# Performance work log

Measured on AMD Instinct MI355X. Metric: run time of the kernel, lower is better.

The kernel has to match this reference:

```python
import jax, jax.numpy as jnp
import numpy as np

HEADS, DIM_HEAD, LANDMARKS, PINV_ITERS = 8, 64, 256, 6
DIM, IN_DIM = 512, 1536
LN_EPS = 1e-5
SCALE = DIM_HEAD ** -0.5


def layernorm(x, g, b):
    mu = x.mean(-1, keepdims=True)
    var = jnp.mean((x - mu) ** 2, axis=-1, keepdims=True)
    return (x - mu) * jax.lax.rsqrt(var + LN_EPS) * g + b


def moore_penrose_pinv(x, iters=PINV_ITERS):
    # Newton-Schulz iteration exactly as in lucidrains/nystrom-attention
    ax = jnp.abs(x)
    z = jnp.swapaxes(x, -1, -2) / (jnp.max(ax.sum(-1)) * jnp.max(ax.sum(-2)))
    I = jnp.eye(x.shape[-1], dtype=x.dtype)
    for _ in range(iters):
        xz = x @ z
        z = 0.25 * z @ (13 * I - xz @ (15 * I - xz @ (7 * I - xz)))
    return z


def nystrom_attention(x, Wqkv, Wout, bout, res_k):
    b, n, _ = x.shape
    m = LANDMARKS
    pad = (m - n % m) % m
    x = jnp.pad(x, ((0, 0), (pad, 0), (0, 0)))  # pad at FRONT like F.pad(..., padding, 0)
    N = n + pad
    qkv = (x @ Wqkv).reshape(b, N, 3, HEADS, DIM_HEAD).transpose(2, 0, 3, 1, 4)
    q, k, v = qkv[0], qkv[1], qkv[2]          # (b, h, N, d)
    q = q * SCALE
    l = N // m
    q_l = q.reshape(b, HEADS, m, l, DIM_HEAD).mean(axis=3)  # landmark pooling
    k_l = k.reshape(b, HEADS, m, l, DIM_HEAD).mean(axis=3)
    attn1 = jax.nn.softmax(jnp.einsum('bhnd,bhmd->bhnm', q, k_l), axis=-1)  # (b,h,N,m)
    attn2 = jax.nn.softmax(jnp.einsum('bhid,bhjd->bhij', q_l, k_l), axis=-1)  # (b,h,m,m)
    attn3 = jax.nn.softmax(jnp.einsum('bhmd,bhnd->bhmn', q_l, k), axis=-1)  # (b,h,m,N)
    out = (attn1 @ moore_penrose_pinv(attn2)) @ (attn3 @ v)  # (b,h,N,d)
    # residual depthwise conv over the sequence dim (kernel 33, per head, no bias)
    res = jax.lax.conv_general_dilated(
        v, res_k, (1, 1), [(16, 16), (0, 0)],
        feature_group_count=HEADS,
        dimension_numbers=('NCHW', 'OIHW', 'NCHW'))
    out = out + res
    out = out.transpose(0, 2, 1, 3).reshape(b, N, HEADS * DIM_HEAD)
    out = out @ Wout + bout
    return out[:, -n:]


def dwconv2d(x, k, bias):
    ph, pw = k.shape[2] // 2, k.shape[3] // 2
    y = jax.lax.conv_general_dilated(
        x, k, (1, 1), [(ph, ph), (pw, pw)],
        feature_group_count=x.shape[1],
        dimension_numbers=('NCHW', 'OIHW', 'NCHW'))
    return y + bias[None, :, None, None]


def ppeg(x, H, W, k7, b7, k5, b5, k3, b3, num_extra=1):
    B, _, C = x.shape
    extra, feat = x[:, :num_extra], x[:, num_extra:]
    cnn = feat.transpose(0, 2, 1).reshape(B, C, H, W)
    y = cnn + dwconv2d(cnn, k7, b7) + dwconv2d(cnn, k5, b5) + dwconv2d(cnn, k3, b3)
    y = y.reshape(B, C, H * W).transpose(0, 2, 1)
    return jnp.concatenate([extra, y], axis=1)


def setup_inputs() -> dict:
    key = jax.random.key(0)
    ks = jax.random.split(key, 16)
    s = 0.02
    d = {
        'features': jax.random.normal(ks[0], (2, 16384, IN_DIM), jnp.float32),
        'W1': jax.random.normal(ks[1], (IN_DIM, DIM), jnp.float32) * s,
        'b1': jnp.zeros((DIM,), jnp.float32),
        'cls': jax.random.normal(ks[2], (1, 1, DIM), jnp.float32),
        'ln1_g': jnp.ones((DIM,), jnp.float32), 'ln1_b': jnp.zeros((DIM,), jnp.float32),
        'Wqkv1': jax.random.normal(ks[3], (DIM, 3 * HEADS * DIM_HEAD), jnp.float32) * s,
        'Wout1': jax.random.normal(ks[4], (HEADS * DIM_HEAD, DIM), jnp.float32) * s,
        'bout1': jnp.zeros((DIM,), jnp.float32),
        'resk1': jax.random.normal(ks[5], (HEADS, 1, 33, 1), jnp.float32) * s,
        'ln2_g': jnp.ones((DIM,), jnp.float32), 'ln2_b': jnp.zeros((DIM,), jnp.float32),
        'Wqkv2': jax.random.normal(ks[6], (DIM, 3 * HEADS * DIM_HEAD), jnp.float32) * s,
        'Wout2': jax.random.normal(ks[7], (HEADS * DIM_HEAD, DIM), jnp.float32) * s,
        'bout2': jnp.zeros((DIM,), jnp.float32),
        'resk2': jax.random.normal(ks[8], (HEADS, 1, 33, 1), jnp.float32) * s,
        'k7': jax.random.normal(ks[9], (DIM, 1, 7, 7), jnp.float32) * s,
        'b7c': jnp.zeros((DIM,), jnp.float32),
        'k5': jax.random.normal(ks[10], (DIM, 1, 5, 5), jnp.float32) * s,
        'b5c': jnp.zeros((DIM,), jnp.float32),
        'k3': jax.random.normal(ks[11], (DIM, 1, 3, 3), jnp.float32) * s,
        'b3c': jnp.zeros((DIM,), jnp.float32),
        'lnf_g': jnp.ones((DIM,), jnp.float32), 'lnf_b': jnp.zeros((DIM,), jnp.float32),
        'W2': jax.random.normal(ks[12], (DIM, 1), jnp.float32) * s,
        'b2': jnp.zeros((1,), jnp.float32),
    }
    return d


def reference(features, W1, b1, cls, ln1_g, ln1_b, Wqkv1, Wout1, bout1, resk1,
              ln2_g, ln2_b, Wqkv2, Wout2, bout2, resk2,
              k7, b7c, k5, b5c, k3, b3c, lnf_g, lnf_b, W2, b2):
    h = jnp.maximum(features @ W1 + b1, 0.0)  # fc1 + ReLU
    Hn = h.shape[1]
    _H = int(np.ceil(np.sqrt(Hn)))
    _W = _H
    add = _H * _W - Hn
    if add > 0:
        h = jnp.concatenate([h, h[:, :add]], axis=1)
    B = h.shape[0]
    cls_tok = jnp.broadcast_to(cls, (B, 1, DIM))
    h = jnp.concatenate([cls_tok, h], axis=1)
    h = h + nystrom_attention(layernorm(h, ln1_g, ln1_b), Wqkv1, Wout1, bout1, resk1)
    h = ppeg(h, _H, _W, k7, b7c, k5, b5c, k3, b3c, num_extra=1)
    h = h + nystrom_attention(layernorm(h, ln2_g, ln2_b), Wqkv2, Wout2, bout2, resk2)
    h = layernorm(h, lnf_g, lnf_b)[:, 0]
    return (h @ W2 + b2).squeeze(-1)  # (B,)
```

## Files before the change

### kernel.cpp

```cpp
#include <hip/hip_runtime.h>
#include <utility>

#define BATCH   2
#define NT      16385
#define NP      16640
#define PADT    255
#define LM      256
#define LAVG    65
#define NHEADS  8
#define DH      64
#define DIM     512
#define INDIM   1536
#define BH      (BATCH*NHEADS)
#define LNEPS   1e-5f
#define QSCALE  0.125f
#define MROWS   (BATCH*NT)
#define MPAD    32896
#define KS3     52
#define KC3     320

typedef _Float16 f16x8_t __attribute__((ext_vector_type(8)));
typedef float    f32x4_t __attribute__((ext_vector_type(4)));

__device__ __forceinline__ void split2(float f, unsigned short& hi, unsigned short& lo) {
// ... 177 lines not shown
__global__ __launch_bounds__(256) void k_outproj_s(
        const unsigned short* __restrict__ Ah, const unsigned short* __restrict__ Al,
        const unsigned short* __restrict__ Bh, const unsigned short* __restrict__ Bl,
        const float* __restrict__ bias, float* __restrict__ hio) {
    MFMA_LDS
    f32x4_t acc[4][4] = {};
    int m0 = blockIdx.y * 128, n0 = blockIdx.x * 128;
    mfma_core_s(Ah, Al, Bh, Bl, DIM, m0, n0, lAh, lAl, lBh, lBl, acc);
    int lane = threadIdx.x & 63, wave = threadIdx.x >> 6;
    int wm = (wave >> 1) * 64, wn = (wave & 1) * 64;
    int c16 = lane & 15, kg = lane >> 4;
#pragma unroll
    for (int i = 0; i < 4; i++)
#pragma unroll
        for (int r = 0; r < 4; r++) {
            int row = m0 + wm + i * 16 + kg * 4 + r;
            if (row >= MROWS) continue;
#pragma unroll
            for (int j = 0; j < 4; j++) {
                int col = n0 + wn + j * 16 + c16;
                hio[(size_t)row * DIM + col] += acc[i][j][r] + bias[col];
            }
        }
}

__global__ __launch_bounds__(256) void k_ln_split(
        const float* __restrict__ x, const float* __restrict__ g,
        const float* __restrict__ bb, unsigned short* __restrict__ yh,
        unsigned short* __restrict__ yl) {
    size_t row = blockIdx.x;
    const float* xr = x + row * DIM;
    int tid = threadIdx.x;
    __shared__ float red[256];
    float v0 = xr[tid], v1 = xr[tid + 256];
    red[tid] = v0 + v1;
    __syncthreads();
    for (int o = 128; o > 0; o >>= 1) { if (tid < o) red[tid] += red[tid + o]; __syncthreads(); }
    float mu = red[0] * (1.0f / DIM);
    __syncthreads();
    float d0 = v0 - mu, d1 = v1 - mu;
    red[tid] = d0 * d0 + d1 * d1;
    __syncthreads();
    for (int o = 128; o > 0; o >>= 1) { if (tid < o) red[tid] += red[tid + o]; __syncthreads(); }
    float rs = rsqrtf(red[0] * (1.0f / DIM) + LNEPS);
    float y0 = d0 * rs * g[tid] + bb[tid];
    float y1 = d1 * rs * g[tid + 256] + bb[tid + 256];
    unsigned short h, l;
    split2(y0, h, l);
    yh[row * DIM + tid] = h; yl[row * DIM + tid] = l;
    split2(y1, h, l);
    yh[row * DIM + tid + 256] = h; yl[row * DIM + tid + 256] = l;
}

__global__ void k_landmark(const float* __restrict__ x, float* __restrict__ xl) {
    int bh = blockIdx.z, i = blockIdx.y, d = threadIdx.x;
    const float* p = x + ((size_t)bh * NP + (size_t)i * LAVG) * DH + d;
    float s = 0.f;
    for (int j = 0; j < LAVG; j++) s += p[(size_t)j * DH];
    xl[((size_t)bh * LM + i) * DH + d] = s * (1.0f / LAVG);
}

__global__ __launch_bounds__(256) void k_scores(
        const float* __restrict__ A, const float* __restrict__ Bm,
        float* __restrict__ C, int Mrows, int Ncols) {
    int bh = blockIdx.z;
    int c0 = blockIdx.x * 64, r0 = blockIdx.y * 64;
    __shared__ float As[64][DH + 1];
    __shared__ float Bs[64][DH + 1];
    int tid = threadIdx.x;
    int tc = tid & 15, tr = tid >> 4;
#pragma unroll
    for (int rep = 0; rep < 4; rep++) {
        int row = rep * 16 + (tid >> 4);
        int c4 = (tid & 15) * 4;
        float4 va = *(const float4*)(A + ((size_t)bh * Mrows + r0 + row) * DH + c4);
        As[row][c4 + 0] = va.x; As[row][c4 + 1] = va.y; As[row][c4 + 2] = va.z; As[row][c4 + 3] = va.w;
        float4 vb = *(const float4*)(Bm + ((size_t)bh * Ncols + c0 + row) * DH + c4);
        Bs[row][c4 + 0] = vb.x; Bs[row][c4 + 1] = vb.y; Bs[row][c4 + 2] = vb.z; Bs[row][c4 + 3] = vb.w;
    }
    __syncthreads();
    float acc[4][4] = {};
#pragma unroll 8
    for (int kk = 0; kk < DH; kk++) {
        float a_[4], b_[4];
#pragma unroll
        for (int i = 0; i < 4; i++) a_[i] = As[tr * 4 + i][kk];
#pragma unroll
        for (int j = 0; j < 4; j++) b_[j] = Bs[tc * 4 + j][kk];
#pragma unroll
        for (int i = 0; i < 4; i++)
#pragma unroll
            for (int j = 0; j < 4; j++) acc[i][j] += a_[i] * b_[j];
    }
#pragma unroll
    for (int i = 0; i < 4; i++)
#pragma unroll
        for (int j = 0; j < 4; j++)
            C[((size_t)bh * Mrows + r0 + tr * 4 + i) * Ncols + c0 + tc * 4 + j] = acc[i][j];
}

__global__ __launch_bounds__(256) void k_softmax(float* __restrict__ S, int len) {
    size_t row = blockIdx.x;
    float* p = S + row * (size_t)len;
    int tid = threadIdx.x;
    __shared__ float red[256];
    float m = -1e30f;
    for (int i = tid; i < len; i += 256) m = fmaxf(m, p[i]);
    red[tid] = m;
    __syncthreads();
    for (int o = 128; o > 0; o >>= 1) { if (tid < o) red[tid] = fmaxf(red[tid], red[tid + o]); __syncthreads(); }
    m = red[0];
    __syncthreads();
// ... 30 lines not shown
    z[((size_t)bh * LM + i) * LM + j] = a2[((size_t)bh * LM + j) * LM + i] * inv;
}

__global__ __launch_bounds__(256) void k_gemm_b64(
        const float* __restrict__ A, const float* __restrict__ Bm, float* __restrict__ C,
        const float* __restrict__ E, int Mr, int Nc, int Kd,
        float alpha, float beta, float dval) {
    int bh = blockIdx.z;
    int r0 = blockIdx.y * 64, c0 = blockIdx.x * 64;
    const float* Ab = A + (size_t)bh * Mr * Kd;
    const float* Bb = Bm + (size_t)bh * Kd * Nc;
    __shared__ float As[64][36];
    __shared__ float Bs[32][68];
    int tid = threadIdx.x;
    int tr = tid >> 4, tc = tid & 15;
    int arw = tid >> 2, ac8 = (tid & 3) * 8;
    int brw = tid >> 3, bc8 = (tid & 7) * 8;
    float acc[4][4] = {};
    for (int k0 = 0; k0 < Kd; k0 += 32) {
        float4 a0 = *(const float4*)(Ab + (size_t)(r0 + arw) * Kd + k0 + ac8);
        float4 a1 = *(const float4*)(Ab + (size_t)(r0 + arw) * Kd + k0 + ac8 + 4);
        *(float4*)&As[arw][ac8] = a0;
        *(float4*)&As[arw][ac8 + 4] = a1;
        float4 b0 = *(const float4*)(Bb + (size_t)(k0 + brw) * Nc + c0 + bc8);
        float4 b1 = *(const float4*)(Bb + (size_t)(k0 + brw) * Nc + c0 + bc8 + 4);
        *(float4*)&Bs[brw][bc8] = b0;
        *(float4*)&Bs[brw][bc8 + 4] = b1;
        __syncthreads();
#pragma unroll
        for (int kk = 0; kk < 32; kk++) {
            float a_[4], b_[4];
#pragma unroll
            for (int i = 0; i < 4; i++) a_[i] = As[tr * 4 + i][kk];
#pragma unroll
            for (int j = 0; j < 4; j++) b_[j] = Bs[kk][tc * 4 + j];
#pragma unroll
            for (int i = 0; i < 4; i++)
#pragma unroll
                for (int j = 0; j < 4; j++) acc[i][j] += a_[i] * b_[j];
        }
        __syncthreads();
    }
#pragma unroll
    for (int i = 0; i < 4; i++)
#pragma unroll
        for (int j = 0; j < 4; j++) {
            int r = r0 + tr * 4 + i, c = c0 + tc * 4 + j;
            float vv = alpha * acc[i][j] + ((r == c) ? dval : 0.f);
            if (E) vv += beta * E[(size_t)bh * Mr * Nc + (size_t)r * Nc + c];
            C[(size_t)bh * Mr * Nc + (size_t)r * Nc + c] = vv;
        }
}

__global__ __launch_bounds__(256, 3) void k_attn3_fused(
        const float* __restrict__ QL, const float* __restrict__ Kg,
        const float* __restrict__ Vg, float* __restrict__ part, float* __restrict__ ml) {
    int ks = blockIdx.x, rt = blockIdx.y, bh = blockIdx.z;
    int r0 = rt * 64;
    __shared__ __align__(16) float Ls[64][68];
    __shared__ __align__(16) float KP[64][68];
    __shared__ __align__(16) float Vs[64][68];
    int tid = threadIdx.x;
    int tr = tid >> 4, tc = tid & 15;
#pragma unroll
    for (int u = 0; u < 4; u++) {
        int idx = tid + u * 256;
        int row = idx >> 4, c4 = (idx & 15) * 4;
        *(float4*)&Ls[row][c4] = *(const float4*)(QL + ((size_t)bh * LM + r0 + row) * DH + c4);
    }
    float m_[4], l_[4];
    f32x4_t o_[4];
#pragma unroll
    for (int i = 0; i < 4; i++) {
        m_[i] = -1e30f; l_[i] = 0.f;
        o_[i] = (f32x4_t){0.f, 0.f, 0.f, 0.f};
    }
    for (int t0 = ks * KC3; t0 < (ks + 1) * KC3; t0 += 64) {
        if (t0 != ks * KC3) __syncthreads();
#pragma unroll
        for (int u = 0; u < 4; u++) {
            int idx = tid + u * 256;
            int row = idx >> 4, c4 = (idx & 15) * 4;
            *(float4*)&KP[row][c4] = *(const float4*)(Kg + ((size_t)bh * NP + t0 + row) * DH + c4);
            *(float4*)&Vs[row][c4] = *(const float4*)(Vg + ((size_t)bh * NP + t0 + row) * DH + c4);
        }
        __syncthreads();
        float s_[4][4] = {};
#pragma unroll
        for (int kk = 0; kk < 64; kk += 4) {
            f32x4_t a4[4], b4[4];
#pragma unroll
            for (int i = 0; i < 4; i++) a4[i] = *(const f32x4_t*)&Ls[tr * 4 + i][kk];
#pragma unroll
            for (int j = 0; j < 4; j++) b4[j] = *(const f32x4_t*)&KP[tc + 16 * j][kk];
#pragma unroll
            for (int i = 0; i < 4; i++)
#pragma unroll
                for (int j = 0; j < 4; j++)
                    s_[i][j] += a4[i].x * b4[j].x + a4[i].y * b4[j].y
                              + a4[i].z * b4[j].z + a4[i].w * b4[j].w;
        }
        __syncthreads();
#pragma unroll
        for (int i = 0; i < 4; i++) {
            float cm = fmaxf(fmaxf(s_[i][0], s_[i][1]), fmaxf(s_[i][2], s_[i][3]));
            cm = fmaxf(cm, __shfl_xor(cm, 1));
            cm = fmaxf(cm, __shfl_xor(cm, 2));
            cm = fmaxf(cm, __shfl_xor(cm, 4));
            cm = fmaxf(cm, __shfl_xor(cm, 8));
            float mn = fmaxf(m_[i], cm);
            float f = __expf(m_[i] - mn);
            float ps = 0.f;
#pragma unroll
            for (int j = 0; j < 4; j++) {
                float p = __expf(s_[i][j] - mn);
                KP[tr * 4 + i][tc + 16 * j] = p;
                ps += p;
            }
            ps += __shfl_xor(ps, 1);
            ps += __shfl_xor(ps, 2);
            ps += __shfl_xor(ps, 4);
            ps += __shfl_xor(ps, 8);
            l_[i] = l_[i] * f + ps;
            m_[i] = mn;
            o_[i] *= f;
        }
        __syncthreads();
#pragma unroll
        for (int kk = 0; kk < 64; kk += 4) {
            f32x4_t p4[4], mv[4];
#pragma unroll
            for (int i = 0; i < 4; i++) p4[i] = *(const f32x4_t*)&KP[tr * 4 + i][kk];
#pragma unroll
            for (int t = 0; t < 4; t++) mv[t] = *(const f32x4_t*)&Vs[kk + t][tc * 4];
#pragma unroll
            for (int i = 0; i < 4; i++)
                o_[i] += p4[i].x * mv[0] + p4[i].y * mv[1] + p4[i].z * mv[2] + p4[i].w * mv[3];
        }
    }
#pragma unroll
    for (int i = 0; i < 4; i++) {
        int r = r0 + tr * 4 + i;
        size_t base = (size_t)(bh * KS3 + ks) * LM + r;
        if (tc == 0) {
            ml[base * 2 + 0] = m_[i];
            ml[base * 2 + 1] = l_[i];
        }
        *(f32x4_t*)&part[base * DH + tc * 4] = o_[i];
    }
}

__global__ void k_attn3_reduce(const float* __restrict__ part, const float* __restrict__ ml,
                               float* __restrict__ a3v) {
    int idx = blockIdx.x * 256 + threadIdx.x;
    if (idx >= BH * LM * DH) return;
    int d = idx & 63;
    int r = (idx >> 6) & (LM - 1);
    int bh = idx >> 14;
    float M = -1e30f;
    for (int ks = 0; ks < KS3; ks++)
        M = fmaxf(M, ml[((size_t)(bh * KS3 + ks) * LM + r) * 2]);
    float L = 0.f, s = 0.f;
    for (int ks = 0; ks < KS3; ks++) {
        size_t base = (size_t)(bh * KS3 + ks) * LM + r;
        float f = __expf(ml[base * 2] - M);
        L += ml[base * 2 + 1] * f;
        s += part[base * DH + d] * f;
    }
    a3v[((size_t)bh * LM + r) * DH + d] = s / L;
}

__global__ __launch_bounds__(256, 3) void k_attn1_fused(
        const float* __restrict__ Qg, const float* __restrict__ KLg,
        const float* __restrict__ M2g, float* __restrict__ attn_out) {
    int tt = blockIdx.x, bh = blockIdx.y;
    int b = bh / NHEADS, hh = bh % NHEADS;
    int tok0 = tt * 64;
    __shared__ __align__(16) float Qs[64][68];
    __shared__ __align__(16) float Bs[64][68];
    __shared__ __align__(16) float Ps[64][68];
    int tid = threadIdx.x;
    int tr = tid >> 4, tc = tid & 15;
#pragma unroll
    for (int u = 0; u < 4; u++) {
        int idx = tid + u * 256;
        int row = idx >> 4, c4 = (idx & 15) * 4;
        int tok = tok0 + row; if (tok >= NT) tok = NT - 1;
        *(float4*)&Qs[row][c4] = *(const float4*)(Qg + ((size_t)bh * NP + tok + PADT) * DH + c4);
    }
    float m_[4], l_[4];
    f32x4_t o_[4];
#pragma unroll
    for (int i = 0; i < 4; i++) {
        m_[i] = -1e30f; l_[i] = 0.f;
        o_[i] = (f32x4_t){0.f, 0.f, 0.f, 0.f};
    }
    for (int ck = 0; ck < 4; ck++) {
        if (ck) __syncthreads();
#pragma unroll
        for (int u = 0; u < 4; u++) {
            int idx = tid + u * 256;
            int row = idx >> 4, c4 = (idx & 15) * 4;
            *(float4*)&Bs[row][c4] =
                *(const float4*)(KLg + ((size_t)bh * LM + ck * 64 + row) * DH + c4);
        }
        __syncthreads();
        float s_[4][4] = {};
#pragma unroll
        for (int kk = 0; kk < 64; kk += 4) {
            f32x4_t a4[4], b4[4];
#pragma unroll
            for (int i = 0; i < 4; i++) a4[i] = *(const f32x4_t*)&Qs[tr * 4 + i][kk];
#pragma unroll
            for (int j = 0; j < 4; j++) b4[j] = *(const f32x4_t*)&Bs[tc + 16 * j][kk];
#pragma unroll
            for (int i = 0; i < 4; i++)
#pragma unroll
                for (int j = 0; j < 4; j++)
                    s_[i][j] += a4[i].x * b4[j].x + a4[i].y * b4[j].y
                              + a4[i].z * b4[j].z + a4[i].w * b4[j].w;
        }
        __syncthreads();
#pragma unroll
        for (int u = 0; u < 4; u++) {
            int idx = tid + u * 256;
            int row = idx >> 4, c4 = (idx & 15) * 4;
            *(float4*)&Bs[row][c4] =
                *(const float4*)(M2g + ((size_t)bh * LM + ck * 64 + row) * DH + c4);
        }
#pragma unroll
        for (int i = 0; i < 4; i++) {
            float cm = fmaxf(fmaxf(s_[i][0], s_[i][1]), fmaxf(s_[i][2], s_[i][3]));
            cm = fmaxf(cm, __shfl_xor(cm, 1));
            cm = fmaxf(cm, __shfl_xor(cm, 2));
            cm = fmaxf(cm, __shfl_xor(cm, 4));
            cm = fmaxf(cm, __shfl_xor(cm, 8));
            float mn = fmaxf(m_[i], cm);
            float f = __expf(m_[i] - mn);
            float ps = 0.f;
#pragma unroll
            for (int j = 0; j < 4; j++) {
                float p = __expf(s_[i][j] - mn);
                Ps[tr * 4 + i][tc + 16 * j] = p;
                ps += p;
            }
            ps += __shfl_xor(ps, 1);
            ps += __shfl_xor(ps, 2);
            ps += __shfl_xor(ps, 4);
            ps += __shfl_xor(ps, 8);
            l_[i] = l_[i] * f + ps;
            m_[i] = mn;
            o_[i] *= f;
        }
        __syncthreads();
#pragma unroll
        for (int kk = 0; kk < 64; kk += 4) {
            f32x4_t p4[4], mv[4];
#pragma unroll
            for (int i = 0; i < 4; i++) p4[i] = *(const f32x4_t*)&Ps[tr * 4 + i][kk];
#pragma unroll
            for (int t = 0; t < 4; t++) mv[t] = *(const f32x4_t*)&Bs[kk + t][tc * 4];
#pragma unroll
            for (int i = 0; i < 4; i++)
                o_[i] += p4[i].x * mv[0] + p4[i].y * mv[1] + p4[i].z * mv[2] + p4[i].w * mv[3];
        }
    }
#pragma unroll
    for (int i = 0; i < 4; i++) {
        int tok = tok0 + tr * 4 + i;
        if (tok >= NT) continue;
        float inv = 1.0f / l_[i];
        f32x4_t r = o_[i] * inv;
        *(f32x4_t*)&attn_out[((size_t)b * NT + tok) * DIM + hh * DH + tc * 4] = r;
    }
}

__global__ __launch_bounds__(256) void k_res_add(
        const float* __restrict__ V, const float* __restrict__ rk, float* __restrict__ attn_out) {
    int bh = blockIdx.y;
    int b = bh / NHEADS, hh = bh % NHEADS;
    int tid = threadIdx.x;
    int tok = blockIdx.x * 4 + (tid >> 6);
    int d = tid & 63;
    __shared__ float k33[33];
    if (tid < 33) k33[tid] = rk[hh * 33 + tid];
    __syncthreads();
    if (tok < NT) {
        int t = tok + PADT;
        float s = 0.f;
#pragma unroll
        for (int u = 0; u < 33; u++) {
            int tp = t - 16 + u;
            if (tp < NP) s += V[((size_t)bh * NP + tp) * DH + d] * k33[u];
        }
        attn_out[((size_t)b * NT + tok) * DIM + hh * DH + d] += s;
    }
}

__global__ void k_combine(const float* __restrict__ k7, const float* __restrict__ b7,
                          const float* __restrict__ k5, const float* __restrict__ b5,
                          const float* __restrict__ k3, const float* __restrict__ b3,
                          float* __restrict__ Kc, float* __restrict__ biasC) {
    int tap = blockIdx.y;
    int c = blockIdx.x * 256 + threadIdx.x;
    if (c >= DIM) return;
    int dy = tap / 7 - 3, dx = tap % 7 - 3;
    int ady = dy < 0 ? -dy : dy, adx = dx < 0 ? -dx : dx;
    float w = k7[(size_t)c * 49 + tap];
    if (ady <= 2 && adx <= 2) w += k5[(size_t)c * 25 + (dy + 2) * 5 + (dx + 2)];
    if (ady <= 1 && adx <= 1) w += k3[(size_t)c * 9 + (dy + 1) * 3 + (dx + 1)];
    if (dy == 0 && dx == 0) w += 1.0f;
    Kc[(size_t)tap * DIM + c] = w;
    if (tap == 0) biasC[c] = b7[c] + b5[c] + b3[c];
}

#define PT 32
#define PH 38
__global__ __launch_bounds__(256) void k_ppeg2(
        const float* __restrict__ h1, const float* __restrict__ Kc,
        const float* __restrict__ biasC, float* __restrict__ h2) {
    int xt = blockIdx.x, yt = blockIdx.y;
    int bz = blockIdx.z;
    int b = bz >> 6, cg = bz & 63, c0 = cg * 8;
    __shared__ __align__(16) float sin2[PH * PH * 8];
    __shared__ __align__(16) float wk2[49 * 8];
    __shared__ float sb[8];
    int tid = threadIdx.x;
    for (int i2 = tid; i2 < 392; i2 += 256) {
        int tap = i2 >> 3, ch = i2 & 7;
// ... 84 lines not shown
        const float* __restrict__ bout, const float* __restrict__ h2, float* __restrict__ h_cls) {
    int b = blockIdx.x, tid = threadIdx.x;
    __shared__ float a[DIM];
    a[tid] = attn_cls[(size_t)b * DIM + tid];
    a[tid + 256] = attn_cls[(size_t)b * DIM + tid + 256];
    __syncthreads();
    for (int c = tid; c < DIM; c += 256) {
        float s = bout[c];
        for (int k2 = 0; k2 < DIM; k2++) s += a[k2] * Wout[(size_t)k2 * DIM + c];
        h_cls[(size_t)b * DIM + c] = h2[(size_t)b * NT * DIM + c] + s;
    }
}

__global__ __launch_bounds__(256) void k_final(
        const float* __restrict__ h_cls, const float* __restrict__ g, const float* __restrict__ bb,
        const float* __restrict__ W2, const float* __restrict__ b2, float* __restrict__ out) {
    int b = blockIdx.x, tid = threadIdx.x;
    const float* x = h_cls + (size_t)b * DIM;
    __shared__ float red[256];
    float v0 = x[tid], v1 = x[tid + 256];
    red[tid] = v0 + v1;
    __syncthreads();
    for (int o = 128; o > 0; o >>= 1) { if (tid < o) red[tid] += red[tid + o]; __syncthreads(); }
    float mu = red[0] * (1.0f / DIM);
    __syncthreads();
    float d0 = v0 - mu, d1 = v1 - mu;
    red[tid] = d0 * d0 + d1 * d1;
    __syncthreads();
    for (int o = 128; o > 0; o >>= 1) { if (tid < o) red[tid] += red[tid + o]; __syncthreads(); }
    float rs = rsqrtf(red[0] * (1.0f / DIM) + LNEPS);
    float y0 = d0 * rs * g[tid] + bb[tid];
    float y1 = d1 * rs * g[tid + 256] + bb[tid + 256];
    red[tid] = y0 * W2[tid] + y1 * W2[tid + 256];
    __syncthreads();
    for (int o = 128; o > 0; o >>= 1) { if (tid < o) red[tid] += red[tid + o]; __syncthreads(); }
    if (tid == 0) out[b] = red[0] + b2[0];
}

struct AttnBufs {
    float *q, *k, *v, *ql, *kl;
    float *a2, *za, *zb, *xz, *ta, *tb;
    float *S, *part, *ml, *a3v, *M2, *scal;
    float *attn_cls, *h_cls;
    unsigned short *actb_h, *actb_l;
};

static void run_attention(hipStream_t stream, const float* hin, float* h_residual,
                          float* attn_out,
                          const float* lng, const float* lnb,
                          const unsigned short* Wqkvt_h, const unsigned short* Wqkvt_l,
                          const unsigned short* Woutt_h, const unsigned short* Woutt_l,
                          const float* Wout_f32, const float* bout,
                          const float* resk, bool full, const AttnBufs& B_) {
    k_ln_split<<<dim3(BATCH * NT), 256, 0, stream>>>(hin, lng, lnb, B_.actb_h, B_.actb_l);
    k_zero_pads<<<dim3((BH * PADT * DH + 255) / 256), 256, 0, stream>>>(B_.q, B_.k, B_.v);
    k_qkv_s<<<dim3(12, MPAD / 128), 256, 0, stream>>>(B_.actb_h, B_.actb_l, Wqkvt_h, Wqkvt_l, B_.q, B_.k, B_.v);
    k_landmark<<<dim3(1, LM, BH), 64, 0, stream>>>(B_.q, B_.ql);
    k_landmark<<<dim3(1, LM, BH), 64, 0, stream>>>(B_.k, B_.kl);
    k_scores<<<dim3(LM / 64, LM / 64, BH), 256, 0, stream>>>(B_.ql, B_.kl, B_.a2, LM, LM);
    k_softmax<<<dim3(BH * LM), 256, 0, stream>>>(B_.a2, LM);
    hipMemsetAsync(B_.scal, 0, 2 * sizeof(float), stream);
    k_pinv_scal<<<dim3(BH), 256, 0, stream>>>(B_.a2, B_.scal);
    k_z0<<<dim3(1, LM, BH), 256, 0, stream>>>(B_.a2, B_.scal, B_.za);
    float* zc = B_.za; float* zn = B_.zb;
    for (int it = 0; it < 6; it++) {
        k_gemm_b64<<<dim3(4, 4, BH), 256, 0, stream>>>(B_.a2, zc, B_.xz, nullptr, LM, LM, LM, 1.f, 0.f, 0.f);
        k_gemm_b64<<<dim3(4, 4, BH), 256, 0, stream>>>(B_.xz, B_.xz, B_.tb, B_.xz, LM, LM, LM, 1.f, -7.f, 15.f);
        k_gemm_b64<<<dim3(4, 4, BH), 256, 0, stream>>>(B_.xz, B_.tb, B_.ta, nullptr, LM, LM, LM, -1.f, 0.f, 13.f);
        k_gemm_b64<<<dim3(4, 4, BH), 256, 0, stream>>>(zc, B_.ta, zn, nullptr, LM, LM, LM, 0.25f, 0.f, 0.f);
        std::swap(zc, zn);
    }
    k_attn3_fused<<<dim3(KS3, LM / 64, BH), 256, 0, stream>>>(B_.ql, B_.k, B_.v, B_.part, B_.ml);
    k_attn3_reduce<<<dim3(BH * LM * DH / 256), 256, 0, stream>>>(B_.part, B_.ml, B_.a3v);
    k_gemm_b64<<<dim3(1, 4, BH), 256, 0, stream>>>(zc, B_.a3v, B_.M2, nullptr, LM, DH, LM, 1.f, 0.f, 0.f);
    if (full) {
        k_attn1_fused<<<dim3((NT + 63) / 64, BH), 256, 0, stream>>>(B_.q, B_.kl, B_.M2, attn_out);
        k_res_add<<<dim3((NT + 3) / 4, BH), 256, 0, stream>>>(B_.v, resk, attn_out);
        k_cvt_split<<<dim3((MROWS * DIM / 4 + 255) / 256), 256, 0, stream>>>(attn_out, B_.actb_h, B_.actb_l, MROWS * DIM / 4);
        k_outproj_s<<<dim3(4, MPAD / 128), 256, 0, stream>>>(B_.actb_h, B_.actb_l, Woutt_h, Woutt_l, bout, h_residual);
    } else {
        k_cls_attn<<<dim3(BH), 256, 0, stream>>>(B_.q, B_.kl, B_.M2, B_.v, resk, B_.attn_cls);
        k_cls_proj<<<dim3(BATCH), 256, 0, stream>>>(B_.attn_cls, Wout_f32, bout, hin, B_.h_cls);
    }
}

extern "C" void kernel_launch(void* const* d_in, const int* in_sizes, int n_in,
                              void* d_out, int out_size, void* d_ws, size_t ws_size,
                              hipStream_t stream) {
    const float* features = (const float*)d_in[0];
    const float* W1    = (const float*)d_in[1];
    const float* b1    = (const float*)d_in[2];
    const float* cls   = (const float*)d_in[3];
    const float* ln1_g = (const float*)d_in[4];
    const float* ln1_b = (const float*)d_in[5];
    const float* Wqkv1 = (const float*)d_in[6];
    const float* Wout1 = (const float*)d_in[7];
    const float* bout1 = (const float*)d_in[8];
    const float* resk1 = (const float*)d_in[9];
    const float* ln2_g = (const float*)d_in[10];
    const float* ln2_b = (const float*)d_in[11];
    const float* Wqkv2 = (const float*)d_in[12];
    const float* Wout2 = (const float*)d_in[13];
    const float* bout2 = (const float*)d_in[14];
    const float* resk2 = (const float*)d_in[15];
    const float* k7    = (const float*)d_in[16];
    const float* b7c   = (const float*)d_in[17];
    const float* k5    = (const float*)d_in[18];
    const float* b5c   = (const float*)d_in[19];
    const float* k3    = (const float*)d_in[20];
    const float* b3c   = (const float*)d_in[21];
    const float* lnf_g = (const float*)d_in[22];
    const float* lnf_b = (const float*)d_in[23];
    const float* W2    = (const float*)d_in[24];
    const float* b2    = (const float*)d_in[25];
    float* out = (float*)d_out;

    float* ws = (float*)d_ws;
    size_t off = 0;
    auto alloc = [&](size_t n) { float* p = ws + off; off += (n + 63) & ~(size_t)63; return p; };
    float* h1  = alloc((size_t)BATCH * NT * DIM);
    float* h2  = alloc((size_t)BATCH * NT * DIM);
    AttnBufs Bu;
    Bu.q    = alloc((size_t)BH * NP * DH);
    Bu.k    = alloc((size_t)BH * NP * DH);
    Bu.v    = alloc((size_t)BH * NP * DH);
    Bu.S    = alloc((size_t)BH * NP * LM);
    Bu.ql   = alloc((size_t)BH * LM * DH);
    Bu.kl   = alloc((size_t)BH * LM * DH);
    Bu.a2   = alloc((size_t)BH * LM * LM);
// ... 47 lines not shown
```

Before: 3.440 ms.

## Port attn1 and attn3 fused softmax-matmul kernels to split-fp16 MFMA

```diff
diff --git a/kernel.cpp b/kernel.cpp
--- a/kernel.cpp
+++ b/kernel.cpp
@@ -253,12 +253,67 @@
     yh[row * DIM + tid + 256] = h; yl[row * DIM + tid + 256] = l;
 }
 
-__global__ void k_landmark(const float* __restrict__ x, float* __restrict__ xl) {
+__global__ void k_landmark(const float* __restrict__ x, float* __restrict__ xl,
+                           unsigned short* __restrict__ xsh, unsigned short* __restrict__ xsl) {
     int bh = blockIdx.z, i = blockIdx.y, d = threadIdx.x;
     const float* p = x + ((size_t)bh * NP + (size_t)i * LAVG) * DH + d;
     float s = 0.f;
     for (int j = 0; j < LAVG; j++) s += p[(size_t)j * DH];
-    xl[((size_t)bh * LM + i) * DH + d] = s * (1.0f / LAVG);
+    float v = s * (1.0f / LAVG);
+    size_t o = ((size_t)bh * LM + i) * DH + d;
+    xl[o] = v;
+    unsigned short h, l; split2(v, h, l);
+    xsh[o] = h; xsl[o] = l;
+}
+
+__global__ __launch_bounds__(256) void k_vt_split(
+        const float* __restrict__ V, unsigned short* __restrict__ Yh,
+        unsigned short* __restrict__ Yl) {
+    int t0 = blockIdx.x * 64, bh = blockIdx.y;
+    __shared__ float tile[64][65];
+    int tid = threadIdx.x;
+#pragma unroll
+    for (int u = 0; u < 4; u++) {
+        int idx = tid + u * 256;
+        int row = idx >> 4, c4 = (idx & 15) * 4;
+        *(float4*)&tile[row][c4] = *(const float4*)(V + ((size_t)bh * NP + t0 + row) * DH + c4);
+    }
+    __syncthreads();
+    int d = tid >> 2, g16 = (tid & 3) * 16;
+    __attribute__((aligned(16))) unsigned short oh[16], ol[16];
+#pragma unroll
+    for (int u = 0; u < 16; u++) split2(tile[g16 + u][d], oh[u], ol[u]);
+    size_t o = ((size_t)bh * DH + d) * NP + t0 + g16;
+#pragma unroll
+    for (int u = 0; u < 4; u++) {
+        *(ushort4*)(Yh + o + u * 4) = *(const ushort4*)&oh[u * 4];
+        *(ushort4*)(Yl + o + u * 4) = *(const ushort4*)&ol[u * 4];
+    }
+}
+
+__global__ __launch_bounds__(256) void k_m2t_split(
+        const float* __restrict__ M2, unsigned short* __restrict__ Yh,
+        unsigned short* __restrict__ Yl) {
+    int l0 = blockIdx.x * 64, bh = blockIdx.y;
+    __shared__ float tile[64][65];
+    int tid = threadIdx.x;
+#pragma unroll
+    for (int u = 0; u < 4; u++) {
+        int idx = tid + u * 256;
+        int row = idx >> 4, c4 = (idx & 15) * 4;
+        *(float4*)&tile[row][c4] = *(const float4*)(M2 + ((size_t)bh * LM + l0 + row) * DH + c4);
+    }
+    __syncthreads();
+    int d = tid >> 2, g16 = (tid & 3) * 16;
+    __attribute__((aligned(16))) unsigned short oh[16], ol[16];
+#pragma unroll
+    for (int u = 0; u < 16; u++) split2(tile[g16 + u][d], oh[u], ol[u]);
+    size_t o = ((size_t)bh * DH + d) * LM + l0 + g16;
+#pragma unroll
+    for (int u = 0; u < 4; u++) {
+        *(ushort4*)(Yh + o + u * 4) = *(const ushort4*)&oh[u * 4];
+        *(ushort4*)(Yl + o + u * 4) = *(const ushort4*)&ol[u * 4];
+    }
 }
 
 __global__ __launch_bounds__(256) void k_scores(
@@ -395,101 +450,254 @@
         }
 }
 
-__global__ __launch_bounds__(256, 3) void k_attn3_fused(
-        const float* __restrict__ QL, const float* __restrict__ Kg,
-        const float* __restrict__ Vg, float* __restrict__ part, float* __restrict__ ml) {
-    int ks = blockIdx.x, rt = blockIdx.y, bh = blockIdx.z;
-    int r0 = rt * 64;
-    __shared__ __align__(16) float Ls[64][68];
-    __shared__ __align__(16) float KP[64][68];
-    __shared__ __align__(16) float Vs[64][68];
+
+__global__ __launch_bounds__(256, 2) void k_attn1_mfma(
+        const unsigned short* __restrict__ qsh, const unsigned short* __restrict__ qsl,
+        const unsigned short* __restrict__ klsh, const unsigned short* __restrict__ klsl,
+        const unsigned short* __restrict__ m2h, const unsigned short* __restrict__ m2l,
+        float* __restrict__ attn_out) {
+    int tt = blockIdx.x, bh = blockIdx.y;
+    int b = bh / NHEADS, hh = bh % NHEADS;
+    int tok0 = tt * 64;
+    __shared__ __align__(16) unsigned short lQh[4096], lQl[4096];
+    __shared__ __align__(16) unsigned short lBh[4096], lBl[4096];
+    __shared__ __align__(16) unsigned short lPh[4096], lPl[4096];
+    __shared__ __align__(16) unsigned short lVh[4096], lVl[4096];
     int tid = threadIdx.x;
-    int tr = tid >> 4, tc = tid & 15;
-#pragma unroll
-    for (int u = 0; u < 4; u++) {
-        int idx = tid + u * 256;
-        int row = idx >> 4, c4 = (idx & 15) * 4;
-        *(float4*)&Ls[row][c4] = *(const float4*)(QL + ((size_t)bh * LM + r0 + row) * DH + c4);
+    int lane = tid & 63, w = tid >> 6;
+    int mrow = lane & 15, kg = lane >> 4;
+    int arow = tid >> 2, acol = (tid & 3) * 8;
+    {
+        int tok = tok0 + arow; if (tok >= NT) tok = NT - 1;
+        size_t src = ((size_t)bh * NP + tok + PADT) * DH + acol;
+        async16(qsh + src,      lQh + tid * 8);
+        async16(qsh + src + 32, lQh + 2048 + tid * 8);
+        async16(qsl + src,      lQl + tid * 8);
+        async16(qsl + src + 32, lQl + 2048 + tid * 8);
     }
     float m_[4], l_[4];
-    f32x4_t o_[4];
-#pragma unroll
-    for (int i = 0; i < 4; i++) {
-        m_[i] = -1e30f; l_[i] = 0.f;
-        o_[i] = (f32x4_t){0.f, 0.f, 0.f, 0.f};
-    }
-    for (int t0 = ks * KC3; t0 < (ks + 1) * KC3; t0 += 64) {
-        if (t0 != ks * KC3) __syncthreads();
-#pragma unroll
-        for (int u = 0; u < 4; u++) {
-            int idx = tid + u * 256;
-            int row = idx >> 4, c4 = (idx & 15) * 4;
-            *(float4*)&KP[row][c4] = *(const float4*)(Kg + ((size_t)bh * NP + t0 + row) * DH + c4);
-            *(float4*)&Vs[row][c4] = *(const float4*)(Vg + ((size_t)bh * NP + t0 + row) * DH + c4);
+    f32x4_t oacc[4];
+#pragma unroll
+    for (int r = 0; r < 4; r++) { m_[r] = -1e30f; l_[r] = 0.f; }
+#pragma unroll
+    for (int j = 0; j < 4; j++) oacc[j] = (f32x4_t){0.f, 0.f, 0.f, 0.f};
+    for (int ck = 0; ck < 4; ck++) {
+        if (ck) __syncthreads();
+        {
+            size_t sb = ((size_t)bh * LM + ck * 64 + arow) * DH + acol;
+            async16(klsh + sb,      lBh + tid * 8);
+            async16(klsh + sb + 32, lBh + 2048 + tid * 8);
+            async16(klsl + sb,      lBl + tid * 8);
+            async16(klsl + sb + 32, lBl + 2048 + tid * 8);
+            size_t sv = ((size_t)bh * DH + arow) * LM + ck * 64 + acol;
+            async16(m2h + sv,      lVh + tid * 8);
+            async16(m2h + sv + 32, lVh + 2048 + tid * 8);
+            async16(m2l + sv,      lVl + tid * 8);
+            async16(m2l + sv + 32, lVl + 2048 + tid * 8);
         }
         __syncthreads();
-        float s_[4][4] = {};
-#pragma unroll
-        for (int kk = 0; kk < 64; kk += 4) {
-            f32x4_t a4[4], b4[4];
-#pragma unroll
-            for (int i = 0; i < 4; i++) a4[i] = *(const f32x4_t*)&Ls[tr * 4 + i][kk];
-#pragma unroll
-            for (int j = 0; j < 4; j++) b4[j] = *(const f32x4_t*)&KP[tc + 16 * j][kk];
-#pragma unroll
-            for (int i = 0; i < 4; i++)
-#pragma unroll
-                for (int j = 0; j < 4; j++)
-                    s_[i][j] += a4[i].x * b4[j].x + a4[i].y * b4[j].y
-                              + a4[i].z * b4[j].z + a4[i].w * b4[j].w;
-        }
-        __syncthreads();
-#pragma unroll
-        for (int i = 0; i < 4; i++) {
-            float cm = fmaxf(fmaxf(s_[i][0], s_[i][1]), fmaxf(s_[i][2], s_[i][3]));
+        f32x4_t acc1[4];
+#pragma unroll
+        for (int j = 0; j < 4; j++) acc1[j] = (f32x4_t){0.f, 0.f, 0.f, 0.f};
+#pragma unroll
+        for (int s = 0; s < 2; s++) {
+            int ao = (s * 64 + w * 16 + mrow) * 32 + kg * 8;
+            f16x8_t ah = *(const f16x8_t*)(lQh + ao);
+            f16x8_t al = *(const f16x8_t*)(lQl + ao);
+#pragma unroll
+            for (int j = 0; j < 4; j++) {
+                int bo = (s * 64 + j * 16 + mrow) * 32 + kg * 8;
+                f16x8_t bhv = *(const f16x8_t*)(lBh + bo);
+                f16x8_t blv = *(const f16x8_t*)(lBl + bo);
+                acc1[j] = __builtin_amdgcn_mfma_f32_16x16x32_f16(ah, bhv, acc1[j], 0, 0, 0);
+                acc1[j] = __builtin_amdgcn_mfma_f32_16x16x32_f16(al, bhv, acc1[j], 0, 0, 0);
+                acc1[j] = __builtin_amdgcn_mfma_f32_16x16x32_f16(ah, blv, acc1[j], 0, 0, 0);
+            }
+        }
+#pragma unroll
+        for (int r = 0; r < 4; r++) {
+            float cm = fmaxf(fmaxf(acc1[0][r], acc1[1][r]), fmaxf(acc1[2][r], acc1[3][r]));
             cm = fmaxf(cm, __shfl_xor(cm, 1));
             cm = fmaxf(cm, __shfl_xor(cm, 2));
             cm = fmaxf(cm, __shfl_xor(cm, 4));
             cm = fmaxf(cm, __shfl_xor(cm, 8));
-            float mn = fmaxf(m_[i], cm);
-            float f = __expf(m_[i] - mn);
-            float ps = 0.f;
-#pragma unroll
-            for (int j = 0; j < 4; j++) {
-                float p = __expf(s_[i][j] - mn);
-                KP[tr * 4 + i][tc + 16 * j] = p;
-                ps += p;
-            }
+            float mn = fmaxf(m_[r], cm);
+            float f = __expf(m_[r] - mn);
+            float p0 = __expf(acc1[0][r] - mn);
+            float p1 = __expf(acc1[1][r] - mn);
+            float p2 = __expf(acc1[2][r] - mn);
+            float p3 = __expf(acc1[3][r] - mn);
+            float ps = p0 + p1 + p2 + p3;
             ps += __shfl_xor(ps, 1);
             ps += __shfl_xor(ps, 2);
             ps += __shfl_xor(ps, 4);
             ps += __shfl_xor(ps, 8);
-            l_[i] = l_[i] * f + ps;
-            m_[i] = mn;
-            o_[i] *= f;
+            l_[r] = l_[r] * f + ps;
+            m_[r] = mn;
+#pragma unroll
+            for (int j = 0; j < 4; j++) oacc[j][r] *= f;
+            int row = w * 16 + kg * 4 + r;
+            float pv[4] = {p0, p1, p2, p3};
+#pragma unroll
+            for (int j = 0; j < 4; j++) {
+                unsigned short ph_, pl_;
+                split2(pv[j], ph_, pl_);
+                int col = j * 16 + mrow;
+                int off = ((col >> 5) * 64 + row) * 32 + (col & 31);
+                lPh[off] = ph_; lPl[off] = pl_;
+            }
         }
         __syncthreads();
 #pragma unroll
-        for (int kk = 0; kk < 64; kk += 4) {
-            f32x4_t p4[4], mv[4];
-#pragma unroll
-            for (int i = 0; i < 4; i++) p4[i] = *(const f32x4_t*)&KP[tr * 4 + i][kk];
-#pragma unroll
-            for (int t = 0; t < 4; t++) mv[t] = *(const f32x4_t*)&Vs[kk + t][tc * 4];
-#pragma unroll
-            for (int i = 0; i < 4; i++)
-                o_[i] += p4[i].x * mv[0] + p4[i].y * mv[1] + p4[i].z * mv[2] + p4[i].w * mv[3];
-        }
-    }
-#pragma unroll
-    for (int i = 0; i < 4; i++) {
-        int r = r0 + tr * 4 + i;
-        size_t base = (size_t)(bh * KS3 + ks) * LM + r;
-        if (tc == 0) {
-            ml[base * 2 + 0] = m_[i];
-            ml[base * 2 + 1] = l_[i];
-        }
-        *(f32x4_t*)&part[base * DH + tc * 4] = o_[i];
+        for (int s = 0; s < 2; s++) {
+            int ao = (s * 64 + w * 16 + mrow) * 32 + kg * 8;
+            f16x8_t ph = *(const f16x8_t*)(lPh + ao);
+            f16x8_t pl = *(const f16x8_t*)(lPl + ao);
+#pragma unroll
+            for (int j = 0; j < 4; j++) {
+                int bo = (s * 64 + j * 16 + mrow) * 32 + kg * 8;
+                f16x8_t vh = *(const f16x8_t*)(lVh + bo);
+                f16x8_t vl = *(const f16x8_t*)(lVl + bo);
+                oacc[j] = __builtin_amdgcn_mfma_f32_16x16x32_f16(ph, vh, oacc[j], 0, 0, 0);
+                oacc[j] = __builtin_amdgcn_mfma_f32_16x16x32_f16(pl, vh, oacc[j], 0, 0, 0);
+                oacc[j] = __builtin_amdgcn_mfma_f32_16x16x32_f16(ph, vl, oacc[j], 0, 0, 0);
+            }
+        }
+    }
+#pragma unroll
+    for (int r = 0; r < 4; r++) {
+        int row = w * 16 + kg * 4 + r;
+        int tok = tok0 + row;
+        if (tok >= NT) continue;
+        float inv = 1.0f / l_[r];
+#pragma unroll
+        for (int j = 0; j < 4; j++)
+            attn_out[((size_t)b * NT + tok) * DIM + hh * DH + j * 16 + mrow] = oacc[j][r] * inv;
+    }
+}
+
+__global__ __launch_bounds__(256, 2) void k_attn3_mfma(
+        const unsigned short* __restrict__ qlh, const unsigned short* __restrict__ qll,
+        const unsigned short* __restrict__ kh, const unsigned short* __restrict__ kl_,
+        const unsigned short* __restrict__ vth, const unsigned short* __restrict__ vtl,
+        float* __restrict__ part, float* __restrict__ ml) {
+    int ks = blockIdx.x, rt = blockIdx.y, bh = blockIdx.z;
+    int r0 = rt * 64;
+    __shared__ __align__(16) unsigned short lQh[4096], lQl[4096];
+    __shared__ __align__(16) unsigned short lBh[4096], lBl[4096];
+    __shared__ __align__(16) unsigned short lPh[4096], lPl[4096];
+    __shared__ __align__(16) unsigned short lVh[4096], lVl[4096];
+    int tid = threadIdx.x;
+    int lane = tid & 63, w = tid >> 6;
+    int mrow = lane & 15, kg = lane >> 4;
+    int arow = tid >> 2, acol = (tid & 3) * 8;
+    {
+        size_t src = ((size_t)bh * LM + r0 + arow) * DH + acol;
+        async16(qlh + src,      lQh + tid * 8);
+        async16(qlh + src + 32, lQh + 2048 + tid * 8);
+        async16(qll + src,      lQl + tid * 8);
+        async16(qll + src + 32, lQl + 2048 + tid * 8);
+    }
+    float m_[4], l_[4];
+    f32x4_t oacc[4];
+#pragma unroll
+    for (int r = 0; r < 4; r++) { m_[r] = -1e30f; l_[r] = 0.f; }
+#pragma unroll
+    for (int j = 0; j < 4; j++) oacc[j] = (f32x4_t){0.f, 0.f, 0.f, 0.f};
+    for (int t0 = ks * KC3; t0 < (ks + 1) * KC3; t0 += 64) {
+        if (t0 != ks * KC3) __syncthreads();
+        {
+            size_t sb = ((size_t)bh * NP + t0 + arow) * DH + acol;
+            async16(kh + sb,       lBh + tid * 8);
+            async16(kh + sb + 32,  lBh + 2048 + tid * 8);
+            async16(kl_ + sb,      lBl + tid * 8);
+            async16(kl_ + sb + 32, lBl + 2048 + tid * 8);
+            size_t sv = ((size_t)bh * DH + arow) * NP + t0 + acol;
+            async16(vth + sv,      lVh + tid * 8);
+            async16(vth + sv + 32, lVh + 2048 + tid * 8);
+            async16(vtl + sv,      lVl + tid * 8);
+            async16(vtl + sv + 32, lVl + 2048 + tid * 8);
+        }
+        __syncthreads();
+        f32x4_t acc1[4];
+#pragma unroll
+        for (int j = 0; j < 4; j++) acc1[j] = (f32x4_t){0.f, 0.f, 0.f, 0.f};
+#pragma unroll
+        for (int s = 0; s < 2; s++) {
+            int ao = (s * 64 + w * 16 + mrow) * 32 + kg * 8;
+            f16x8_t ah = *(const f16x8_t*)(lQh + ao);
+            f16x8_t al = *(const f16x8_t*)(lQl + ao);
+#pragma unroll
+            for (int j = 0; j < 4; j++) {
+                int bo = (s * 64 + j * 16 + mrow) * 32 + kg * 8;
+                f16x8_t bhv = *(const f16x8_t*)(lBh + bo);
+                f16x8_t blv = *(const f16x8_t*)(lBl + bo);
+                acc1[j] = __builtin_amdgcn_mfma_f32_16x16x32_f16(ah, bhv, acc1[j], 0, 0, 0);
+                acc1[j] = __builtin_amdgcn_mfma_f32_16x16x32_f16(al, bhv, acc1[j], 0, 0, 0);
+                acc1[j] = __builtin_amdgcn_mfma_f32_16x16x32_f16(ah, blv, acc1[j], 0, 0, 0);
+            }
+        }
+#pragma unroll
+        for (int r = 0; r < 4; r++) {
+            float cm = fmaxf(fmaxf(acc1[0][r], acc1[1][r]), fmaxf(acc1[2][r], acc1[3][r]));
+            cm = fmaxf(cm, __shfl_xor(cm, 1));
+            cm = fmaxf(cm, __shfl_xor(cm, 2));
+            cm = fmaxf(cm, __shfl_xor(cm, 4));
+            cm = fmaxf(cm, __shfl_xor(cm, 8));
+            float mn = fmaxf(m_[r], cm);
+            float f = __expf(m_[r] - mn);
+            float p0 = __expf(acc1[0][r] - mn);
+            float p1 = __expf(acc1[1][r] - mn);
+            float p2 = __expf(acc1[2][r] - mn);
+            float p3 = __expf(acc1[3][r] - mn);
+            float ps = p0 + p1 + p2 + p3;
+            ps += __shfl_xor(ps, 1);
+            ps += __shfl_xor(ps, 2);
+            ps += __shfl_xor(ps, 4);
+            ps += __shfl_xor(ps, 8);
+            l_[r] = l_[r] * f + ps;
+            m_[r] = mn;
+#pragma unroll
+            for (int j = 0; j < 4; j++) oacc[j][r] *= f;
+            int row = w * 16 + kg * 4 + r;
+            float pv[4] = {p0, p1, p2, p3};
+#pragma unroll
+            for (int j = 0; j < 4; j++) {
+                unsigned short ph_, pl_;
+                split2(pv[j], ph_, pl_);
+                int col = j * 16 + mrow;
+                int off = ((col >> 5) * 64 + row) * 32 + (col & 31);
+                lPh[off] = ph_; lPl[off] = pl_;
+            }
+        }
+        __syncthreads();
+#pragma unroll
+        for (int s = 0; s < 2; s++) {
+            int ao = (s * 64 + w * 16 + mrow) * 32 + kg * 8;
+            f16x8_t ph = *(const f16x8_t*)(lPh + ao);
+            f16x8_t pl = *(const f16x8_t*)(lPl + ao);
+#pragma unroll
+            for (int j = 0; j < 4; j++) {
+                int bo = (s * 64 + j * 16 + mrow) * 32 + kg * 8;
+                f16x8_t vh = *(const f16x8_t*)(lVh + bo);
+                f16x8_t vl = *(const f16x8_t*)(lVl + bo);
+                oacc[j] = __builtin_amdgcn_mfma_f32_16x16x32_f16(ph, vh, oacc[j], 0, 0, 0);
+                oacc[j] = __builtin_amdgcn_mfma_f32_16x16x32_f16(pl, vh, oacc[j], 0, 0, 0);
+                oacc[j] = __builtin_amdgcn_mfma_f32_16x16x32_f16(ph, vl, oacc[j], 0, 0, 0);
+            }
+        }
+    }
+#pragma unroll
+    for (int r = 0; r < 4; r++) {
+        int rg = r0 + w * 16 + kg * 4 + r;
+        size_t base = (size_t)(bh * KS3 + ks) * LM + rg;
+        if (mrow == 0) {
+            ml[base * 2 + 0] = m_[r];
+            ml[base * 2 + 1] = l_[r];
+        }
+#pragma unroll
+        for (int j = 0; j < 4; j++)
+            part[base * DH + j * 16 + mrow] = oacc[j][r];
     }
 }
 
@@ -513,111 +721,6 @@
     a3v[((size_t)bh * LM + r) * DH + d] = s / L;
 }
 
-__global__ __launch_bounds__(256, 3) void k_attn1_fused(
-        const float* __restrict__ Qg, const float* __restrict__ KLg,
-        const float* __restrict__ M2g, float* __restrict__ attn_out) {
-    int tt = blockIdx.x, bh = blockIdx.y;
-    int b = bh / NHEADS, hh = bh % NHEADS;
-    int tok0 = tt * 64;
-    __shared__ __align__(16) float Qs[64][68];
-    __shared__ __align__(16) float Bs[64][68];
-    __shared__ __align__(16) float Ps[64][68];
-    int tid = threadIdx.x;
-    int tr = tid >> 4, tc = tid & 15;
-#pragma unroll
-    for (int u = 0; u < 4; u++) {
-        int idx = tid + u * 256;
-        int row = idx >> 4, c4 = (idx & 15) * 4;
-        int tok = tok0 + row; if (tok >= NT) tok = NT - 1;
-        *(float4*)&Qs[row][c4] = *(const float4*)(Qg + ((size_t)bh * NP + tok + PADT) * DH + c4);
-    }
-    float m_[4], l_[4];
-    f32x4_t o_[4];
-#pragma unroll
-    for (int i = 0; i < 4; i++) {
-        m_[i] = -1e30f; l_[i] = 0.f;
-        o_[i] = (f32x4_t){0.f, 0.f, 0.f, 0.f};
-    }
-    for (int ck = 0; ck < 4; ck++) {
-        if (ck) __syncthreads();
-#pragma unroll
-        for (int u = 0; u < 4; u++) {
-            int idx = tid + u * 256;
-            int row = idx >> 4, c4 = (idx & 15) * 4;
-            *(float4*)&Bs[row][c4] =
-                *(const float4*)(KLg + ((size_t)bh * LM + ck * 64 + row) * DH + c4);
-        }
-        __syncthreads();
-        float s_[4][4] = {};
-#pragma unroll
-        for (int kk = 0; kk < 64; kk += 4) {
-            f32x4_t a4[4], b4[4];
-#pragma unroll
-            for (int i = 0; i < 4; i++) a4[i] = *(const f32x4_t*)&Qs[tr * 4 + i][kk];
-#pragma unroll
-            for (int j = 0; j < 4; j++) b4[j] = *(const f32x4_t*)&Bs[tc + 16 * j][kk];
-#pragma unroll
-            for (int i = 0; i < 4; i++)
-#pragma unroll
-                for (int j = 0; j < 4; j++)
-                    s_[i][j] += a4[i].x * b4[j].x + a4[i].y * b4[j].y
-                              + a4[i].z * b4[j].z + a4[i].w * b4[j].w;
-        }
-        __syncthreads();
-#pragma unroll
-        for (int u = 0; u < 4; u++) {
-            int idx = tid + u * 256;
-            int row = idx >> 4, c4 = (idx & 15) * 4;
-            *(float4*)&Bs[row][c4] =
-                *(const float4*)(M2g + ((size_t)bh * LM + ck * 64 + row) * DH + c4);
-        }
-#pragma unroll
-        for (int i = 0; i < 4; i++) {
-            float cm = fmaxf(fmaxf(s_[i][0], s_[i][1]), fmaxf(s_[i][2], s_[i][3]));
-            cm = fmaxf(cm, __shfl_xor(cm, 1));
-            cm = fmaxf(cm, __shfl_xor(cm, 2));
-            cm = fmaxf(cm, __shfl_xor(cm, 4));
-            cm = fmaxf(cm, __shfl_xor(cm, 8));
-            float mn = fmaxf(m_[i], cm);
-            float f = __expf(m_[i] - mn);
-            float ps = 0.f;
-#pragma unroll
-            for (int j = 0; j < 4; j++) {
-                float p = __expf(s_[i][j] - mn);
-                Ps[tr * 4 + i][tc + 16 * j] = p;
-                ps += p;
-            }
-            ps += __shfl_xor(ps, 1);
-            ps += __shfl_xor(ps, 2);
-            ps += __shfl_xor(ps, 4);
-            ps += __shfl_xor(ps, 8);
-            l_[i] = l_[i] * f + ps;
-            m_[i] = mn;
-            o_[i] *= f;
-        }
-        __syncthreads();
-#pragma unroll
-        for (int kk = 0; kk < 64; kk += 4) {
-            f32x4_t p4[4], mv[4];
-#pragma unroll
-            for (int i = 0; i < 4; i++) p4[i] = *(const f32x4_t*)&Ps[tr * 4 + i][kk];
-#pragma unroll
-            for (int t = 0; t < 4; t++) mv[t] = *(const f32x4_t*)&Bs[kk + t][tc * 4];
-#pragma unroll
-            for (int i = 0; i < 4; i++)
-                o_[i] += p4[i].x * mv[0] + p4[i].y * mv[1] + p4[i].z * mv[2] + p4[i].w * mv[3];
-        }
-    }
-#pragma unroll
-    for (int i = 0; i < 4; i++) {
-        int tok = tok0 + tr * 4 + i;
-        if (tok >= NT) continue;
-        float inv = 1.0f / l_[i];
-        f32x4_t r = o_[i] * inv;
-        *(f32x4_t*)&attn_out[((size_t)b * NT + tok) * DIM + hh * DH + tc * 4] = r;
-    }
-}
-
 __global__ __launch_bounds__(256) void k_res_add(
         const float* __restrict__ V, const float* __restrict__ rk, float* __restrict__ attn_out) {
     int bh = blockIdx.y;
@@ -808,11 +911,27 @@
                           const unsigned short* Woutt_h, const unsigned short* Woutt_l,
                           const float* Wout_f32, const float* bout,
                           const float* resk, bool full, const AttnBufs& B_) {
+    unsigned short* sp = (unsigned short*)B_.S;
+    auto su = [&](size_t n) { unsigned short* p = sp; sp += (n + 63) & ~(size_t)63; return p; };
+    const size_t NQ = (size_t)BH * NP * DH;
+    const size_t NL = (size_t)BH * LM * DH;
+    unsigned short *qsh = su(NQ), *qsl = su(NQ);
+    unsigned short *ksh = su(NQ), *ksl = su(NQ);
+    unsigned short *vth = su(NQ), *vtl = su(NQ);
+    unsigned short *qlsh = su(NL), *qlsl = su(NL);
+    unsigned short *klsh = su(NL), *klsl = su(NL);
+    unsigned short *m2th = su(NL), *m2tl = su(NL);
+
     k_ln_split<<<dim3(BATCH * NT), 256, 0, stream>>>(hin, lng, lnb, B_.actb_h, B_.actb_l);
     k_zero_pads<<<dim3((BH * PADT * DH + 255) / 256), 256, 0, stream>>>(B_.q, B_.k, B_.v);
     k_qkv_s<<<dim3(12, MPAD / 128), 256, 0, stream>>>(B_.actb_h, B_.actb_l, Wqkvt_h, Wqkvt_l, B_.q, B_.k, B_.v);
-    k_landmark<<<dim3(1, LM, BH), 64, 0, stream>>>(B_.q, B_.ql);
-    k_landmark<<<dim3(1, LM, BH), 64, 0, stream>>>(B_.k, B_.kl);
+    const int NQ4 = BH * NP * DH / 4;
+    if (full)
+        k_cvt_split<<<dim3((NQ4 + 255) / 256), 256, 0, stream>>>(B_.q, qsh, qsl, NQ4);
+    k_cvt_split<<<dim3((NQ4 + 255) / 256), 256, 0, stream>>>(B_.k, ksh, ksl, NQ4);
+    k_vt_split<<<dim3(NP / 64, BH), 256, 0, stream>>>(B_.v, vth, vtl);
+    k_landmark<<<dim3(1, LM, BH), 64, 0, stream>>>(B_.q, B_.ql, qlsh, qlsl);
+    k_landmark<<<dim3(1, LM, BH), 64, 0, stream>>>(B_.k, B_.kl, klsh, klsl);
     k_scores<<<dim3(LM / 64, LM / 64, BH), 256, 0, stream>>>(B_.ql, B_.kl, B_.a2, LM, LM);
     k_softmax<<<dim3(BH * LM), 256, 0, stream>>>(B_.a2, LM);
     hipMemsetAsync(B_.scal, 0, 2 * sizeof(float), stream);
@@ -826,11 +945,12 @@
         k_gemm_b64<<<dim3(4, 4, BH), 256, 0, stream>>>(zc, B_.ta, zn, nullptr, LM, LM, LM, 0.25f, 0.f, 0.f);
         std::swap(zc, zn);
     }
-    k_attn3_fused<<<dim3(KS3, LM / 64, BH), 256, 0, stream>>>(B_.ql, B_.k, B_.v, B_.part, B_.ml);
+    k_attn3_mfma<<<dim3(KS3, LM / 64, BH), 256, 0, stream>>>(qlsh, qlsl, ksh, ksl, vth, vtl, B_.part, B_.ml);
     k_attn3_reduce<<<dim3(BH * LM * DH / 256), 256, 0, stream>>>(B_.part, B_.ml, B_.a3v);
     k_gemm_b64<<<dim3(1, 4, BH), 256, 0, stream>>>(zc, B_.a3v, B_.M2, nullptr, LM, DH, LM, 1.f, 0.f, 0.f);
     if (full) {
-        k_attn1_fused<<<dim3((NT + 63) / 64, BH), 256, 0, stream>>>(B_.q, B_.kl, B_.M2, attn_out);
+        k_m2t_split<<<dim3(LM / 64, BH), 256, 0, stream>>>(B_.M2, m2th, m2tl);
+        k_attn1_mfma<<<dim3((NT + 63) / 64, BH), 256, 0, stream>>>(qsh, qsl, klsh, klsl, m2th, m2tl, attn_out);
         k_res_add<<<dim3((NT + 3) / 4, BH), 256, 0, stream>>>(B_.v, resk, attn_out);
         k_cvt_split<<<dim3((MROWS * DIM / 4 + 255) / 256), 256, 0, stream>>>(attn_out, B_.actb_h, B_.actb_l, MROWS * DIM / 4);
         k_outproj_s<<<dim3(4, MPAD / 128), 256, 0, stream>>>(B_.actb_h, B_.actb_l, Woutt_h, Woutt_l, bout, h_residual);
```

Result: faster. 2.997 ms (-12.9%).
